# Optimization experiments

Measured on AMD Instinct MI355X. Metric: run time of the kernel, lower is better.

The kernel has to match this reference:

```python
import jax, jax.numpy as jnp
import numpy as np

NUM_HEADS = 6
ROPE_BASE = 10000.0


def _rope_cos_sin(T, head_dim, dtype):
    # Llama-style rotary embedding tables: [T, head_dim]
    inv_freq = 1.0 / (ROPE_BASE ** (jnp.arange(0, head_dim, 2, dtype=jnp.float32) / head_dim))
    pos = jnp.arange(T, dtype=jnp.float32)
    freqs = pos[:, None] * inv_freq[None, :]          # [T, head_dim//2]
    emb = jnp.concatenate([freqs, freqs], axis=-1)    # [T, head_dim]
    return jnp.cos(emb).astype(dtype), jnp.sin(emb).astype(dtype)


def _rotate_half(x):
    h = x.shape[-1] // 2
    return jnp.concatenate([-x[..., h:], x[..., :h]], axis=-1)


def setup_inputs() -> dict:
    key = jax.random.key(0)
    k0, k1, k2 = jax.random.split(key, 3)
    N, T, D = 8, 2048, 384
    x = jax.random.normal(k0, (N, T, D), dtype=jnp.float32)
    Wqkv = jax.random.normal(k1, (3 * D, D), dtype=jnp.float32) * 0.02
    Wout = jax.random.normal(k2, (D, D), dtype=jnp.float32) * 0.02
    return {"x": x, "Wqkv": Wqkv, "Wout": Wout}


def reference(x, Wqkv, Wout):
    N, T, D = x.shape
    H = NUM_HEADS
    hd = D // H

    qkv = jnp.einsum('ntd,ed->nte', x, Wqkv)          # [N, T, 3D]
    q, k, v = jnp.split(qkv, 3, axis=-1)

    def heads(t):  # [N,T,D] -> [N,H,T,hd]
        return t.reshape(N, T, H, hd).transpose(0, 2, 1, 3)

    q, k, v = heads(q), heads(k), heads(v)

    cos, sin = _rope_cos_sin(T, hd, x.dtype)          # [T, hd]
    cos = cos[None, None]                              # [1,1,T,hd]
    sin = sin[None, None]
    q = q * cos + _rotate_half(q) * sin
    k = k * cos + _rotate_half(k) * sin

    scale = 1.0 / jnp.sqrt(jnp.asarray(hd, x.dtype))
    scores = jnp.einsum('nhqd,nhkd->nhqk', q, k) * scale
    causal = jnp.tril(jnp.ones((T, T), dtype=bool))
    scores = jnp.where(causal[None, None], scores, jnp.asarray(-jnp.inf, x.dtype))
    attn = jax.nn.softmax(scores, axis=-1)
    ctx = jnp.einsum('nhqk,nhkd->nhqd', attn, v)      # [N,H,T,hd]
    ctx = ctx.transpose(0, 2, 1, 3).reshape(N, T, D)
    return jnp.einsum('ntd,ed->nte', ctx, Wout)
```

## Files before the change

### kernel.cpp

```cpp
#include <hip/hip_runtime.h>
#include <math.h>

#define NB 8
#define TS 2048
#define DM 384
#define NH 6
#define HD 64
#define E3 1152
#define MROWS (NB*TS)

typedef __attribute__((ext_vector_type(8))) short bf16x8;
typedef __attribute__((ext_vector_type(4))) float f32x4;

__device__ __forceinline__ ushort f2bf(float f) {
    uint u = __float_as_uint(f);
    uint r = (u + 0x7FFFu + ((u >> 16) & 1u)) >> 16;
    return (ushort)r;
}
__device__ __forceinline__ float bf2f(ushort h) {
    return __uint_as_float(((uint)h) << 16);
}

#define GL_LDS16(gp, lp) \
  __builtin_amdgcn_global_load_lds((const __attribute__((address_space(1))) uint32_t*)(gp), \
                                   (__attribute__((address_space(3))) uint32_t*)(lp), 16, 0, 0)

__global__ void rope_table_k(float* __restrict__ cosT, float* __restrict__ sinT) {
    int i = blockIdx.x * 256 + threadIdx.x;
    if (i >= TS * HD) return;
    int t   = i >> 6;
    int idx = i & 63;
    int fi  = idx & 31;
    float inv = expf(-(float)fi * (logf(10000.0f) * (1.0f / 32.0f)));
    float ang = (float)t * inv;
    cosT[i] = cosf(ang);
    sinT[i] = sinf(ang);
}

__global__ __launch_bounds__(256) void qkv_mfma_k(
    const float* __restrict__ X, const float* __restrict__ W,
    const float* __restrict__ cosT, const float* __restrict__ sinT,
    ushort* __restrict__ Qhi, ushort* __restrict__ Qlo,
    ushort* __restrict__ Khi, ushort* __restrict__ Klo,
    ushort* __restrict__ Vthi, ushort* __restrict__ Vtlo) {
    __shared__ __align__(16) char smem[49152];
    ushort* Ah = (ushort*)smem;
    ushort* Al = Ah + 128 * 64;
    ushort* Bh = Al + 128 * 64;
    ushort* Bl = Bh + 64 * 64;
    float*  VT = (float*)smem;

    const int tid  = threadIdx.x;
    const int w    = tid >> 6;
    const int lane = tid & 63;
    const int g    = lane >> 4;
    const int c    = lane & 15;
    const int row0 = blockIdx.x * 128;
    const int col0 = blockIdx.y * 64;

    f32x4 acc[2][4];
    #pragma unroll
    for (int mf = 0; mf < 2; ++mf)
        #pragma unroll
        for (int nf = 0; nf < 4; ++nf) acc[mf][nf] = (f32x4){0.f, 0.f, 0.f, 0.f};

    const int srow  = tid >> 1;
    const int shalf = tid & 1;
    const int fra   = (srow ^ (srow >> 3)) & 7;

    for (int kt = 0; kt < 6; ++kt) {
        const int k0 = kt * 64;
        float xv[32];
        {
            const float* xp = &X[(size_t)(row0 + srow) * DM + k0 + shalf * 32];
            #pragma unroll
            for (int j = 0; j < 8; ++j) {
                float4 t4 = *(const float4*)(xp + j * 4);
                xv[j*4+0] = t4.x; xv[j*4+1] = t4.y; xv[j*4+2] = t4.z; xv[j*4+3] = t4.w;
            }
        }
        float wv[32];
        if (tid < 128) {
            const float* wp = &W[(size_t)(col0 + srow) * DM + k0 + shalf * 32];
            #pragma unroll
            for (int j = 0; j < 8; ++j) {
                float4 t4 = *(const float4*)(wp + j * 4);
                wv[j*4+0] = t4.x; wv[j*4+1] = t4.y; wv[j*4+2] = t4.z; wv[j*4+3] = t4.w;
            }
        }
        __syncthreads();
        #pragma unroll
        for (int ch4 = 0; ch4 < 4; ++ch4) {
            bf16x8 hv, lv;
            #pragma unroll
            for (int e = 0; e < 8; ++e) {
                float f = xv[ch4 * 8 + e];
                ushort h = f2bf(f);
                hv[e] = (short)h;
                lv[e] = (short)f2bf(f - bf2f(h));
            }
            int off = srow * 64 + (((shalf * 4 + ch4) ^ fra) << 3);
            *(bf16x8*)&Ah[off] = hv;
            *(bf16x8*)&Al[off] = lv;
        }
        if (tid < 128) {
            #pragma unroll
            for (int ch4 = 0; ch4 < 4; ++ch4) {
                bf16x8 hv, lv;
                #pragma unroll
                for (int e = 0; e < 8; ++e) {
                    float f = wv[ch4 * 8 + e];
                    ushort h = f2bf(f);
                    hv[e] = (short)h;
                    lv[e] = (short)f2bf(f - bf2f(h));
                }
                int off = srow * 64 + (((shalf * 4 + ch4) ^ fra) << 3);
                *(bf16x8*)&Bh[off] = hv;
                *(bf16x8*)&Bl[off] = lv;
            }
        }
        __syncthreads();
        bf16x8 ahf[2][2], alf[2][2], bhf[4][2], blf[4][2];
        #pragma unroll
        for (int mf = 0; mf < 2; ++mf) {
            int arow = w * 32 + mf * 16 + c;
            int fa = (arow ^ (arow >> 3)) & 7;
            #pragma unroll
            for (int kf = 0; kf < 2; ++kf) {
                int off = arow * 64 + (((kf * 4 + g) ^ fa) << 3);
                ahf[mf][kf] = *(const bf16x8*)&Ah[off];
                alf[mf][kf] = *(const bf16x8*)&Al[off];
            }
        }
        #pragma unroll
        for (int nf = 0; nf < 4; ++nf) {
            int brow = nf * 16 + c;
            int fb = (brow ^ (brow >> 3)) & 7;
            #pragma unroll
            for (int kf = 0; kf < 2; ++kf) {
                int off = brow * 64 + (((kf * 4 + g) ^ fb) << 3);
                bhf[nf][kf] = *(const bf16x8*)&Bh[off];
                blf[nf][kf] = *(const bf16x8*)&Bl[off];
            }
        }
        __builtin_amdgcn_s_setprio(1);
        #pragma unroll
        for (int mf = 0; mf < 2; ++mf)
            #pragma unroll
            for (int nf = 0; nf < 4; ++nf)
                #pragma unroll
                for (int kf = 0; kf < 2; ++kf) {
                    acc[mf][nf] = __builtin_amdgcn_mfma_f32_16x16x32_bf16(ahf[mf][kf], bhf[nf][kf], acc[mf][nf], 0, 0, 0);
                    acc[mf][nf] = __builtin_amdgcn_mfma_f32_16x16x32_bf16(alf[mf][kf], bhf[nf][kf], acc[mf][nf], 0, 0, 0);
                    acc[mf][nf] = __builtin_amdgcn_mfma_f32_16x16x32_bf16(ahf[mf][kf], blf[nf][kf], acc[mf][nf], 0, 0, 0);
                }
        __builtin_amdgcn_s_setprio(0);
    }

    const int which = blockIdx.y / 6;
    const int hh    = blockIdx.y % 6;
    const int n     = row0 >> 11;
    const int nh    = n * NH + hh;

    if (which < 2) {
        ushort* dhi = (which == 0) ? Qhi : Khi;
        ushort* dlo = (which == 0) ? Qlo : Klo;
        const float qs = (which == 0) ? 0.125f : 1.0f;
        #pragma unroll
        for (int mf = 0; mf < 2; ++mf)
            #pragma unroll
            for (int r = 0; r < 4; ++r) {
                int t = (row0 + w * 32 + mf * 16 + 4 * g + r) & (TS - 1);
                #pragma unroll
                for (int nf = 0; nf < 4; ++nf) {
                    int p = nf * 16 + c;
                    float a = acc[mf][nf][r];
                    float b = acc[mf][nf ^ 2][r];
                    float cc = cosT[t * HD + p];
                    float ss = sinT[t * HD + p];
                    float v = (nf < 2) ? (a * cc - b * ss) : (a * cc + b * ss);
                    v *= qs;
                    ushort h = f2bf(v);
                    size_t addr = ((size_t)nh * TS + t) * HD + p;
                    dhi[addr] = h;
                    dlo[addr] = f2bf(v - bf2f(h));
                }
            }
    } else {
        __syncthreads();
        #pragma unroll
        for (int mf = 0; mf < 2; ++mf)
            #pragma unroll
            for (int nf = 0; nf < 4; ++nf)
                #pragma unroll
                for (int r = 0; r < 4; ++r)
                    VT[(nf * 16 + c) * 132 + w * 32 + mf * 16 + 4 * g + r] = acc[mf][nf][r];
        __syncthreads();
        int d = tid >> 2, seg = (tid & 3) * 32;
        int t0 = row0 & (TS - 1);
        size_t vbase = ((size_t)nh * HD + d) * TS + t0 + seg;
        #pragma unroll
        for (int j = 0; j < 4; ++j) {
            bf16x8 hv, lv;
            #pragma unroll
            for (int e = 0; e < 8; ++e) {
                float f = VT[d * 132 + seg + j * 8 + e];
                ushort h = f2bf(f);
                hv[e] = (short)h;
                lv[e] = (short)f2bf(f - bf2f(h));
            }
            *(bf16x8*)&Vthi[vbase + j * 8] = hv;
            *(bf16x8*)&Vtlo[vbase + j * 8] = lv;
        }
    }
}

__global__ __launch_bounds__(256) void flash_mfma_k(
    const ushort* __restrict__ Qhi, const ushort* __restrict__ Qlo,
    const ushort* __restrict__ Khi_g, const ushort* __restrict__ Klo_g,
    const ushort* __restrict__ Vthi_g, const ushort* __restrict__ Vtlo_g,
    ushort* __restrict__ ctxhi, ushort* __restrict__ ctxlo) {
    __shared__ ushort Kh[2][2048], Kl[2][2048];
    __shared__ ushort Vh[2][2048], Vl[2][2048];
    __shared__ uint   Pw[4][2][320];

    const int tid  = threadIdx.x;
    const int w    = tid >> 6;
    const int lane = tid & 63;
    const int g    = lane >> 4;
    const int c    = lane & 15;

    const int b   = blockIdx.x;
    const int xcd = b & 7;
    const int li  = b >> 3;
    const int nh  = xcd * 6 + li / 8;
    const int pr  = li % 8;
    const int qtA = 15 - pr, qtB = pr;

    const int kkey = tid >> 3, kcid = tid & 7;
    const ushort* khs = Khi_g + (size_t)nh * TS * HD + (size_t)kkey * HD + ((kcid ^ (kkey & 7)) << 3);
    const ushort* kls = Klo_g + (size_t)nh * TS * HD + (size_t)kkey * HD + ((kcid ^ (kkey & 7)) << 3);
    const int vd = tid >> 2, vkc = (tid & 3) ^ ((vd >> 1) & 3);
    const ushort* vhs = Vthi_g + ((size_t)nh * HD + vd) * TS + vkc * 8;
    const ushort* vls = Vtlo_g + ((size_t)nh * HD + vd) * TS + vkc * 8;
    const int ldsoff = w << 9;

    #define STAGE(buf, kt) do {                                   \
        size_t ko = (size_t)(kt) * (32 * HD);                     \
        int    vo = (kt) * 32;                                    \
        GL_LDS16(khs + ko, &Kh[buf][ldsoff]);                     \
        GL_LDS16(kls + ko, &Kl[buf][ldsoff]);                     \
        GL_LDS16(vhs + vo, &Vh[buf][ldsoff]);                     \
        GL_LDS16(vls + vo, &Vl[buf][ldsoff]);                     \
    } while (0)

    const int n2 = nh / NH, hh2 = nh % NH;

    for (int ph = 0; ph < 2; ++ph) {
        const int qt = ph ? qtB : qtA;
        const int qrow0 = qt * 128 + w * 32;
        const int nkt = 4 * qt + 4;
        const int wave_last = 4 * qt + w;

        bf16x8 qh[2][2], ql[2][2];
        #pragma unroll
        for (int mf = 0; mf < 2; ++mf)
            #pragma unroll
            for (int kf = 0; kf < 2; ++kf) {
                size_t a = ((size_t)nh * TS + qrow0 + mf * 16 + c) * HD + kf * 32 + g * 8;
                qh[mf][kf] = *(const bf16x8*)&Qhi[a];
                ql[mf][kf] = *(const bf16x8*)&Qlo[a];
            }

        f32x4 o[4][2];
        float mr[2], lr[2];
        #pragma unroll
        for (int vnf = 0; vnf < 4; ++vnf)
            #pragma unroll
            for (int mf = 0; mf < 2; ++mf) o[vnf][mf] = (f32x4){0.f, 0.f, 0.f, 0.f};
        mr[0] = mr[1] = -INFINITY;
        lr[0] = lr[1] = 0.f;

        STAGE(0, 0);
        __syncthreads();
        int buf = 0;

        for (int kt = 0; kt < nkt; ++kt) {
            if (kt + 1 < nkt) STAGE(buf ^ 1, kt + 1);

            if (kt <= wave_last) {
                bf16x8 khf[2][2], klf[2][2];
                #pragma unroll
                for (int knf = 0; knf < 2; ++knf)
                    #pragma unroll
                    for (int kf = 0; kf < 2; ++kf) {
                        int key = knf * 16 + c;
                        int off = key * 64 + ((kf * 32 + g * 8) ^ ((key & 7) << 3));
                        khf[knf][kf] = *(const bf16x8*)&Kh[buf][off];
                        klf[knf][kf] = *(const bf16x8*)&Kl[buf][off];
                    }

                f32x4 st[2][2];
                __builtin_amdgcn_s_setprio(1);
                #pragma unroll
                for (int knf = 0; knf < 2; ++knf)
                    #pragma unroll
                    for (int mf = 0; mf < 2; ++mf) {
                        f32x4 a2 = (f32x4){0.f, 0.f, 0.f, 0.f};
                        #pragma unroll
                        for (int kf = 0; kf < 2; ++kf) {
                            a2 = __builtin_amdgcn_mfma_f32_16x16x32_bf16(khf[knf][kf], qh[mf][kf], a2, 0, 0, 0);
                            a2 = __builtin_amdgcn_mfma_f32_16x16x32_bf16(khf[knf][kf], ql[mf][kf], a2, 0, 0, 0);
                            a2 = __builtin_amdgcn_mfma_f32_16x16x32_bf16(klf[knf][kf], qh[mf][kf], a2, 0, 0, 0);
                        }
                        st[knf][mf] = a2;
                    }
                __builtin_amdgcn_s_setprio(0);

                if (kt == wave_last) {
                    #pragma unroll
                    for (int knf = 0; knf < 2; ++knf)
                        #pragma unroll
                        for (int mf = 0; mf < 2; ++mf)
                            #pragma unroll
                            for (int r = 0; r < 4; ++r) {
                                int key = kt * 32 + knf * 16 + 4 * g + r;
                                int q   = qrow0 + mf * 16 + c;
                                if (key > q) st[knf][mf][r] = -INFINITY;
                            }
                }

                #pragma unroll
                for (int mf = 0; mf < 2; ++mf) {
                    float tm = st[0][mf][0];
                    #pragma unroll
                    for (int r = 1; r < 4; ++r) tm = fmaxf(tm, st[0][mf][r]);
                    #pragma unroll
                    for (int r = 0; r < 4; ++r) tm = fmaxf(tm, st[1][mf][r]);
                    tm = fmaxf(tm, __shfl_xor(tm, 16));
                    tm = fmaxf(tm, __shfl_xor(tm, 32));
                    float nm   = fmaxf(mr[mf], tm);
                    float corr = __expf(mr[mf] - nm);
                    mr[mf] = nm;

                    float rs = 0.f;
                    uint wrd[2][2];
                    #pragma unroll
                    for (int knf = 0; knf < 2; ++knf)
                        #pragma unroll
                        for (int h = 0; h < 2; ++h) {
                            float p0 = __expf(st[knf][mf][2*h]   - nm);
                            float p1 = __expf(st[knf][mf][2*h+1] - nm);
                            ushort b0 = f2bf(p0), b1 = f2bf(p1);
                            wrd[knf][h] = (uint)b0 | ((uint)b1 << 16);
                            rs += bf2f(b0) + bf2f(b1);
                        }
                    rs += __shfl_xor(rs, 16);
                    rs += __shfl_xor(rs, 32);
                    lr[mf] = lr[mf] * corr + rs;
                    #pragma unroll
                    for (int vnf = 0; vnf < 4; ++vnf)
                        #pragma unroll
                        for (int r = 0; r < 4; ++r) o[vnf][mf][r] *= corr;

                    uint* pl = &Pw[w][mf][0];
                    #pragma unroll
                    for (int knf = 0; knf < 2; ++knf)
                        #pragma unroll
                        for (int h = 0; h < 2; ++h)
                            pl[c * 20 + 8 * knf + 2 * g + h] = wrd[knf][h];
                }

                bf16x8 pa[2];
                #pragma unroll
                for (int mf = 0; mf < 2; ++mf)
                    pa[mf] = *(const bf16x8*)&Pw[w][mf][c * 20 + 4 * g];

                bf16x8 vhf[4], vlf[4];
                #pragma unroll
                for (int vnf = 0; vnf < 4; ++vnf) {
                    int d = vnf * 16 + c;
                    int off = d * 32 + ((g ^ ((d >> 1) & 3)) << 3);
                    vhf[vnf] = *(const bf16x8*)&Vh[buf][off];
                    vlf[vnf] = *(const bf16x8*)&Vl[buf][off];
                }
                __builtin_amdgcn_s_setprio(1);
                #pragma unroll
                for (int vnf = 0; vnf < 4; ++vnf)
                    #pragma unroll
                    for (int mf = 0; mf < 2; ++mf) {
                        o[vnf][mf] = __builtin_amdgcn_mfma_f32_16x16x32_bf16(vhf[vnf], pa[mf], o[vnf][mf], 0, 0, 0);
                        o[vnf][mf] = __builtin_amdgcn_mfma_f32_16x16x32_bf16(vlf[vnf], pa[mf], o[vnf][mf], 0, 0, 0);
                    }
                __builtin_amdgcn_s_setprio(0);
            }

            __syncthreads();
            buf ^= 1;
        }

        #pragma unroll
        for (int mf = 0; mf < 2; ++mf) {
            float inv = 1.0f / lr[mf];
            int q = qrow0 + mf * 16 + c;
            size_t rowb = ((size_t)(n2 * TS + q)) * DM + hh2 * HD;
            #pragma unroll
            for (int vnf = 0; vnf < 4; ++vnf) {
                ushort4 hv, lv;
                #pragma unroll
                for (int r = 0; r < 4; ++r) {
                    float v = o[vnf][mf][r] * inv;
                    ushort h = f2bf(v);
                    ((ushort*)&hv)[r] = h;
                    ((ushort*)&lv)[r] = f2bf(v - bf2f(h));
                }
                *(ushort4*)&ctxhi[rowb + vnf * 16 + 4 * g] = hv;
                *(ushort4*)&ctxlo[rowb + vnf * 16 + 4 * g] = lv;
            }
        }
    }
    #undef STAGE
}

__global__ __launch_bounds__(256) void outproj_mfma_k(
    const ushort* __restrict__ Ahi_g, const ushort* __restrict__ Alo_g,
    const float* __restrict__ W, float* __restrict__ out) {
    __shared__ __align__(16) char smem[49152];
    ushort* Ah = (ushort*)smem;
    ushort* Al = Ah + 128 * 64;
    ushort* Bh = Al + 128 * 64;
    ushort* Bl = Bh + 64 * 64;

    const int tid  = threadIdx.x;
    const int w    = tid >> 6;
    const int lane = tid & 63;
    const int g    = lane >> 4;
    const int c    = lane & 15;
    const int row0 = blockIdx.x * 128;
    const int col0 = blockIdx.y * 64;

    f32x4 acc[2][4];
    #pragma unroll
    for (int mf = 0; mf < 2; ++mf)
        #pragma unroll
        for (int nf = 0; nf < 4; ++nf) acc[mf][nf] = (f32x4){0.f, 0.f, 0.f, 0.f};

    const int srow  = tid >> 1;
    const int shalf = tid & 1;
    const int fra   = (srow ^ (srow >> 3)) & 7;

    for (int kt = 0; kt < 6; ++kt) {
        const int k0 = kt * 64;
        bf16x8 ahv[4], alv[4];
        {
            const ushort* ap = &Ahi_g[(size_t)(row0 + srow) * DM + k0 + shalf * 32];
            const ushort* lp = &Alo_g[(size_t)(row0 + srow) * DM + k0 + shalf * 32];
            #pragma unroll
            for (int j = 0; j < 4; ++j) {
                ahv[j] = *(const bf16x8*)(ap + j * 8);
                alv[j] = *(const bf16x8*)(lp + j * 8);
            }
        }
        float wv[32];
        if (tid < 128) {
            const float* wp = &W[(size_t)(col0 + srow) * DM + k0 + shalf * 32];
            #pragma unroll
            for (int j = 0; j < 8; ++j) {
                float4 t4 = *(const float4*)(wp + j * 4);
                wv[j*4+0] = t4.x; wv[j*4+1] = t4.y; wv[j*4+2] = t4.z; wv[j*4+3] = t4.w;
            }
        }
        __syncthreads();
        #pragma unroll
        for (int j = 0; j < 4; ++j) {
            int off = srow * 64 + (((shalf * 4 + j) ^ fra) << 3);
            *(bf16x8*)&Ah[off] = ahv[j];
            *(bf16x8*)&Al[off] = alv[j];
        }
        if (tid < 128) {
            #pragma unroll
            for (int ch4 = 0; ch4 < 4; ++ch4) {
                bf16x8 hv, lv;
                #pragma unroll
                for (int e = 0; e < 8; ++e) {
                    float f = wv[ch4 * 8 + e];
                    ushort h = f2bf(f);
                    hv[e] = (short)h;
                    lv[e] = (short)f2bf(f - bf2f(h));
                }
                int off = srow * 64 + (((shalf * 4 + ch4) ^ fra) << 3);
                *(bf16x8*)&Bh[off] = hv;
                *(bf16x8*)&Bl[off] = lv;
            }
        }
        __syncthreads();
        bf16x8 ahf[2][2], alf[2][2], bhf[4][2], blf[4][2];
        #pragma unroll
        for (int mf = 0; mf < 2; ++mf) {
            int arow = w * 32 + mf * 16 + c;
            int fa = (arow ^ (arow >> 3)) & 7;
            #pragma unroll
            for (int kf = 0; kf < 2; ++kf) {
                int off = arow * 64 + (((kf * 4 + g) ^ fa) << 3);
                ahf[mf][kf] = *(const bf16x8*)&Ah[off];
                alf[mf][kf] = *(const bf16x8*)&Al[off];
            }
        }
        #pragma unroll
        for (int nf = 0; nf < 4; ++nf) {
            int brow = nf * 16 + c;
            int fb = (brow ^ (brow >> 3)) & 7;
            #pragma unroll
            for (int kf = 0; kf < 2; ++kf) {
                int off = brow * 64 + (((kf * 4 + g) ^ fb) << 3);
                bhf[nf][kf] = *(const bf16x8*)&Bh[off];
                blf[nf][kf] = *(const bf16x8*)&Bl[off];
            }
        }
        __builtin_amdgcn_s_setprio(1);
        #pragma unroll
        for (int mf = 0; mf < 2; ++mf)
            #pragma unroll
            for (int nf = 0; nf < 4; ++nf)
                #pragma unroll
                for (int kf = 0; kf < 2; ++kf) {
                    acc[mf][nf] = __builtin_amdgcn_mfma_f32_16x16x32_bf16(ahf[mf][kf], bhf[nf][kf], acc[mf][nf], 0, 0, 0);
                    acc[mf][nf] = __builtin_amdgcn_mfma_f32_16x16x32_bf16(alf[mf][kf], bhf[nf][kf], acc[mf][nf], 0, 0, 0);
                    acc[mf][nf] = __builtin_amdgcn_mfma_f32_16x16x32_bf16(ahf[mf][kf], blf[nf][kf], acc[mf][nf], 0, 0, 0);
                }
        __builtin_amdgcn_s_setprio(0);
    }

    #pragma unroll
    for (int mf = 0; mf < 2; ++mf)
        #pragma unroll
        for (int r = 0; r < 4; ++r) {
            int row = row0 + w * 32 + mf * 16 + 4 * g + r;
            #pragma unroll
            for (int nf = 0; nf < 4; ++nf)
                out[(size_t)row * DM + col0 + nf * 16 + c] = acc[mf][nf][r];
        }
}

extern "C" void kernel_launch(void* const* d_in, const int* in_sizes, int n_in,
                              void* d_out, int out_size, void* d_ws, size_t ws_size,
                              hipStream_t stream) {
    const float* x    = (const float*)d_in[0];
    const float* Wqkv = (const float*)d_in[1];
    const float* Wout = (const float*)d_in[2];
    float* out = (float*)d_out;

    const size_t NHT = (size_t)NB * NH * TS * HD;
    char* ws = (char*)d_ws;
    float* cosT = (float*)ws;                        ws += TS * HD * 4;
    float* sinT = (float*)ws;                        ws += TS * HD * 4;
    ushort* Qhi = (ushort*)ws;                       ws += NHT * 2;
    ushort* Qlo = (ushort*)ws;                       ws += NHT * 2;
    ushort* Khi = (ushort*)ws;                       ws += NHT * 2;
    ushort* Klo = (ushort*)ws;                       ws += NHT * 2;
    ushort* Vthi = (ushort*)ws;                      ws += NHT * 2;
    ushort* Vtlo = (ushort*)ws;                      ws += NHT * 2;
    ushort* ctxhi = (ushort*)ws;                     ws += (size_t)MROWS * DM * 2;
    ushort* ctxlo = (ushort*)ws;                     ws += (size_t)MROWS * DM * 2;

    rope_table_k<<<(TS * HD) / 256, 256, 0, stream>>>(cosT, sinT);
    qkv_mfma_k<<<dim3(MROWS / 128, E3 / 64), 256, 0, stream>>>(
        x, Wqkv, cosT, sinT, Qhi, Qlo, Khi, Klo, Vthi, Vtlo);
    flash_mfma_k<<<384, 256, 0, stream>>>(
        Qhi, Qlo, Khi, Klo, Vthi, Vtlo, ctxhi, ctxlo);
    outproj_mfma_k<<<dim3(MROWS / 128, DM / 64), 256, 0, stream>>>(
        ctxhi, ctxlo, Wout, out);
}
```

Measured before the change: 372.8 us.

## Pre-split inputs and weights into bf16 hi/lo and skip redundant softmax rescale

Adds a pre-pass kernel that splits x, Wqkv and Wout into bf16 hi/lo halves once, so the GEMM kernels load ready bf16 tiles instead of converting fp32 in every block (the QKV GEMM previously reconverted each x tile 18 times across column blocks). The x split reuses the ctx buffers as scratch. The flash kernel also skips the running-max correction and rescaling of the accumulator when no lane's row max increased. In exchange there is an extra kernel launch and an extra write and read of the split x in global memory.

```diff
diff --git a/kernel.cpp b/kernel.cpp
--- a/kernel.cpp
+++ b/kernel.cpp
@@ -24,6 +24,35 @@
 #define GL_LDS16(gp, lp) \
   __builtin_amdgcn_global_load_lds((const __attribute__((address_space(1))) uint32_t*)(gp), \
                                    (__attribute__((address_space(3))) uint32_t*)(lp), 16, 0, 0)
+
+__global__ void split_hilo_k(const float* __restrict__ X,
+                             const float* __restrict__ Wq,
+                             const float* __restrict__ Wo,
+                             ushort* __restrict__ Xhi, ushort* __restrict__ Xlo,
+                             ushort* __restrict__ Wqhi, ushort* __restrict__ Wqlo,
+                             ushort* __restrict__ Wohi, ushort* __restrict__ Wolo) {
+    const int NX = MROWS * DM / 4;
+    const int NQ = E3 * DM / 4;
+    const int NO = DM * DM / 4;
+    const int total = NX + NQ + NO;
+    for (int idx = blockIdx.x * 256 + threadIdx.x; idx < total; idx += gridDim.x * 256) {
+        const float* src; ushort* dh; ushort* dl; int i;
+        if (idx < NX)           { src = X;  dh = Xhi;  dl = Xlo;  i = idx; }
+        else if (idx < NX + NQ) { src = Wq; dh = Wqhi; dl = Wqlo; i = idx - NX; }
+        else                    { src = Wo; dh = Wohi; dl = Wolo; i = idx - NX - NQ; }
+        float4 v = *(const float4*)&src[(size_t)i * 4];
+        float f[4] = {v.x, v.y, v.z, v.w};
+        ushort4 hv, lv;
+        #pragma unroll
+        for (int j = 0; j < 4; ++j) {
+            ushort h = f2bf(f[j]);
+            ((ushort*)&hv)[j] = h;
+            ((ushort*)&lv)[j] = f2bf(f[j] - bf2f(h));
+        }
+        *(ushort4*)&dh[(size_t)i * 4] = hv;
+        *(ushort4*)&dl[(size_t)i * 4] = lv;
+    }
+}
 
 __global__ void rope_table_k(float* __restrict__ cosT, float* __restrict__ sinT) {
     int i = blockIdx.x * 256 + threadIdx.x;
@@ -38,7 +67,8 @@
 }
 
 __global__ __launch_bounds__(256) void qkv_mfma_k(
-    const float* __restrict__ X, const float* __restrict__ W,
+    const ushort* __restrict__ Xhi_g, const ushort* __restrict__ Xlo_g,
+    const ushort* __restrict__ Whi_g, const ushort* __restrict__ Wlo_g,
     const float* __restrict__ cosT, const float* __restrict__ sinT,
     ushort* __restrict__ Qhi, ushort* __restrict__ Qlo,
     ushort* __restrict__ Khi, ushort* __restrict__ Klo,
@@ -70,53 +100,39 @@
 
     for (int kt = 0; kt < 6; ++kt) {
         const int k0 = kt * 64;
-        float xv[32];
+        bf16x8 xav[4], xlv[4];
         {
-            const float* xp = &X[(size_t)(row0 + srow) * DM + k0 + shalf * 32];
-            #pragma unroll
-            for (int j = 0; j < 8; ++j) {
-                float4 t4 = *(const float4*)(xp + j * 4);
-                xv[j*4+0] = t4.x; xv[j*4+1] = t4.y; xv[j*4+2] = t4.z; xv[j*4+3] = t4.w;
-            }
-        }
-        float wv[32];
+            const ushort* ap = &Xhi_g[(size_t)(row0 + srow) * DM + k0 + shalf * 32];
+            const ushort* lp = &Xlo_g[(size_t)(row0 + srow) * DM + k0 + shalf * 32];
+            #pragma unroll
+            for (int j = 0; j < 4; ++j) {
+                xav[j] = *(const bf16x8*)(ap + j * 8);
+                xlv[j] = *(const bf16x8*)(lp + j * 8);
+            }
+        }
+        bf16x8 wav[4], wlv[4];
         if (tid < 128) {
-            const float* wp = &W[(size_t)(col0 + srow) * DM + k0 + shalf * 32];
-            #pragma unroll
-            for (int j = 0; j < 8; ++j) {
-                float4 t4 = *(const float4*)(wp + j * 4);
-                wv[j*4+0] = t4.x; wv[j*4+1] = t4.y; wv[j*4+2] = t4.z; wv[j*4+3] = t4.w;
-            }
-        }
-        __syncthreads();
-        #pragma unroll
-        for (int ch4 = 0; ch4 < 4; ++ch4) {
-            bf16x8 hv, lv;
-            #pragma unroll
-            for (int e = 0; e < 8; ++e) {
-                float f = xv[ch4 * 8 + e];
-                ushort h = f2bf(f);
-                hv[e] = (short)h;
-                lv[e] = (short)f2bf(f - bf2f(h));
-            }
-            int off = srow * 64 + (((shalf * 4 + ch4) ^ fra) << 3);
-            *(bf16x8*)&Ah[off] = hv;
-            *(bf16x8*)&Al[off] = lv;
+            const ushort* ap = &Whi_g[(size_t)(col0 + srow) * DM + k0 + shalf * 32];
+            const ushort* lp = &Wlo_g[(size_t)(col0 + srow) * DM + k0 + shalf * 32];
+            #pragma unroll
+            for (int j = 0; j < 4; ++j) {
+                wav[j] = *(const bf16x8*)(ap + j * 8);
+                wlv[j] = *(const bf16x8*)(lp + j * 8);
+            }
+        }
+        __syncthreads();
+        #pragma unroll
+        for (int j = 0; j < 4; ++j) {
+            int off = srow * 64 + (((shalf * 4 + j) ^ fra) << 3);
+            *(bf16x8*)&Ah[off] = xav[j];
+            *(bf16x8*)&Al[off] = xlv[j];
         }
         if (tid < 128) {
             #pragma unroll
-            for (int ch4 = 0; ch4 < 4; ++ch4) {
-                bf16x8 hv, lv;
-                #pragma unroll
-                for (int e = 0; e < 8; ++e) {
-                    float f = wv[ch4 * 8 + e];
-                    ushort h = f2bf(f);
-                    hv[e] = (short)h;
-                    lv[e] = (short)f2bf(f - bf2f(h));
-                }
-                int off = srow * 64 + (((shalf * 4 + ch4) ^ fra) << 3);
-                *(bf16x8*)&Bh[off] = hv;
-                *(bf16x8*)&Bl[off] = lv;
+            for (int j = 0; j < 4; ++j) {
+                int off = srow * 64 + (((shalf * 4 + j) ^ fra) << 3);
+                *(bf16x8*)&Bh[off] = wav[j];
+                *(bf16x8*)&Bl[off] = wlv[j];
             }
         }
         __syncthreads();
@@ -339,9 +355,17 @@
                     for (int r = 0; r < 4; ++r) tm = fmaxf(tm, st[1][mf][r]);
                     tm = fmaxf(tm, __shfl_xor(tm, 16));
                     tm = fmaxf(tm, __shfl_xor(tm, 32));
-                    float nm   = fmaxf(mr[mf], tm);
-                    float corr = __expf(mr[mf] - nm);
-                    mr[mf] = nm;
+                    if (!__all(tm <= mr[mf])) {
+                        float nm   = fmaxf(mr[mf], tm);
+                        float corr = __expf(mr[mf] - nm);
+                        mr[mf] = nm;
+                        lr[mf] *= corr;
+                        #pragma unroll
+                        for (int vnf = 0; vnf < 4; ++vnf)
+                            #pragma unroll
+                            for (int r = 0; r < 4; ++r) o[vnf][mf][r] *= corr;
+                    }
+                    const float nm = mr[mf];
 
                     float rs = 0.f;
                     uint wrd[2][2];
@@ -357,11 +381,7 @@
                         }
                     rs += __shfl_xor(rs, 16);
                     rs += __shfl_xor(rs, 32);
-                    lr[mf] = lr[mf] * corr + rs;
-                    #pragma unroll
-                    for (int vnf = 0; vnf < 4; ++vnf)
-                        #pragma unroll
-                        for (int r = 0; r < 4; ++r) o[vnf][mf][r] *= corr;
+                    lr[mf] += rs;
 
                     uint* pl = &Pw[w][mf][0];
                     #pragma unroll
@@ -424,7 +444,8 @@
 
 __global__ __launch_bounds__(256) void outproj_mfma_k(
     const ushort* __restrict__ Ahi_g, const ushort* __restrict__ Alo_g,
-    const float* __restrict__ W, float* __restrict__ out) {
+    const ushort* __restrict__ Whi_g, const ushort* __restrict__ Wlo_g,
+    float* __restrict__ out) {
     __shared__ __align__(16) char smem[49152];
     ushort* Ah = (ushort*)smem;
     ushort* Al = Ah + 128 * 64;
@@ -461,13 +482,14 @@
                 alv[j] = *(const bf16x8*)(lp + j * 8);
             }
         }
-        float wv[32];
+        bf16x8 wav[4], wlv[4];
         if (tid < 128) {
-            const float* wp = &W[(size_t)(col0 + srow) * DM + k0 + shalf * 32];
-            #pragma unroll
-            for (int j = 0; j < 8; ++j) {
-                float4 t4 = *(const float4*)(wp + j * 4);
-                wv[j*4+0] = t4.x; wv[j*4+1] = t4.y; wv[j*4+2] = t4.z; wv[j*4+3] = t4.w;
+            const ushort* ap = &Whi_g[(size_t)(col0 + srow) * DM + k0 + shalf * 32];
+            const ushort* lp = &Wlo_g[(size_t)(col0 + srow) * DM + k0 + shalf * 32];
+            #pragma unroll
+            for (int j = 0; j < 4; ++j) {
+                wav[j] = *(const bf16x8*)(ap + j * 8);
+                wlv[j] = *(const bf16x8*)(lp + j * 8);
             }
         }
         __syncthreads();
@@ -479,18 +501,10 @@
         }
         if (tid < 128) {
             #pragma unroll
-            for (int ch4 = 0; ch4 < 4; ++ch4) {
-                bf16x8 hv, lv;
-                #pragma unroll
-                for (int e = 0; e < 8; ++e) {
-                    float f = wv[ch4 * 8 + e];
-                    ushort h = f2bf(f);
-                    hv[e] = (short)h;
-                    lv[e] = (short)f2bf(f - bf2f(h));
-                }
-                int off = srow * 64 + (((shalf * 4 + ch4) ^ fra) << 3);
-                *(bf16x8*)&Bh[off] = hv;
-                *(bf16x8*)&Bl[off] = lv;
+            for (int j = 0; j < 4; ++j) {
+                int off = srow * 64 + (((shalf * 4 + j) ^ fra) << 3);
+                *(bf16x8*)&Bh[off] = wav[j];
+                *(bf16x8*)&Bl[off] = wlv[j];
             }
         }
         __syncthreads();
@@ -562,12 +576,20 @@
     ushort* Vtlo = (ushort*)ws;                      ws += NHT * 2;
     ushort* ctxhi = (ushort*)ws;                     ws += (size_t)MROWS * DM * 2;
     ushort* ctxlo = (ushort*)ws;                     ws += (size_t)MROWS * DM * 2;
-
+    ushort* Wqhi = (ushort*)ws;                      ws += (size_t)E3 * DM * 2;
+    ushort* Wqlo = (ushort*)ws;                      ws += (size_t)E3 * DM * 2;
+    ushort* Wohi = (ushort*)ws;                      ws += (size_t)DM * DM * 2;
+    ushort* Wolo = (ushort*)ws;                      ws += (size_t)DM * DM * 2;
+    ushort* Xhi = ctxhi;
+    ushort* Xlo = ctxlo;
+
+    split_hilo_k<<<2048, 256, 0, stream>>>(x, Wqkv, Wout,
+        Xhi, Xlo, Wqhi, Wqlo, Wohi, Wolo);
     rope_table_k<<<(TS * HD) / 256, 256, 0, stream>>>(cosT, sinT);
     qkv_mfma_k<<<dim3(MROWS / 128, E3 / 64), 256, 0, stream>>>(
-        x, Wqkv, cosT, sinT, Qhi, Qlo, Khi, Klo, Vthi, Vtlo);
+        Xhi, Xlo, Wqhi, Wqlo, cosT, sinT, Qhi, Qlo, Khi, Klo, Vthi, Vtlo);
     flash_mfma_k<<<384, 256, 0, stream>>>(
         Qhi, Qlo, Khi, Klo, Vthi, Vtlo, ctxhi, ctxlo);
-    outproj_mfma_k<<<dim3(MROWS / 128, DM / 64), 256, 0, stream>>>(
-        ctxhi, ctxlo, Wout, out);
-}
+    outproj_mfma_k<<<dim3(MROWS / 128, DM / 6 / 64 * 6), 256, 0, stream>>>(
+        ctxhi, ctxlo, Wohi, Wolo, out);
+}
```

New measurement: 330.9 us. 11.2% less time.
